# Performance work log

Measured on AMD Instinct MI355X. Metric: run time of the kernel, lower is better.

## Reference

```python
import jax, jax.numpy as jnp
import numpy as np

N_NODES = 10000
N_EDGES = 320000
N_GRAPHS = 64
IN_DIM = 1
HID = 256


def setup_inputs() -> dict:
    key = jax.random.key(0)
    ks = jax.random.split(key, 12)
    s = 1.0 / np.sqrt(HID)
    inp = {
        "x": jax.random.normal(ks[0], (N_NODES, IN_DIM), dtype=jnp.float32),
        "edge_index": jax.random.randint(ks[1], (2, N_EDGES), 0, N_NODES, dtype=jnp.int64),
        "batch": jnp.sort(jax.random.randint(ks[2], (N_NODES,), 0, N_GRAPHS, dtype=jnp.int64)),
        "W_emb": jax.random.normal(ks[3], (IN_DIM, HID), dtype=jnp.float32),
        "b_emb": jnp.zeros((HID,), dtype=jnp.float32),
        "W1a": jax.random.normal(ks[4], (HID, HID), dtype=jnp.float32) * s,
        "b1a": jnp.zeros((HID,), dtype=jnp.float32),
        "W1b": jax.random.normal(ks[5], (HID, HID), dtype=jnp.float32) * s,
        "b1b": jnp.zeros((HID,), dtype=jnp.float32),
        "W2a": jax.random.normal(ks[6], (HID, HID), dtype=jnp.float32) * s,
        "b2a": jnp.zeros((HID,), dtype=jnp.float32),
        "W2b": jax.random.normal(ks[7], (HID, HID), dtype=jnp.float32) * s,
        "b2b": jnp.zeros((HID,), dtype=jnp.float32),
    }
    return inp


def _pointnet_conv(h, src, dst, Wa, ba, Wb, bb):
    # gather x_j -> 2-layer MLP per edge -> scatter-max at dst (PyG aggr='max')
    msg = jax.nn.relu(h[src] @ Wa + ba) @ Wb + bb          # [E, HID]
    agg = jax.ops.segment_max(msg, dst, num_segments=N_NODES)
    # PyG fills nodes with no incoming messages with 0
    return jnp.where(jnp.isneginf(agg), 0.0, agg)


def reference(x, edge_index, batch, W_emb, b_emb, W1a, b1a, W1b, b1b, W2a, b2a, W2b, b2b):
    src, dst = edge_index[0], edge_index[1]
    h = jax.nn.silu(x @ W_emb + b_emb)                     # [N, HID]
    h = h + jax.nn.silu(_pointnet_conv(h, src, dst, W1a, b1a, W1b, b1b))
    h = h + jax.nn.silu(_pointnet_conv(h, src, dst, W2a, b2a, W2b, b2b))
    # global_mean_pool over graphs
    sums = jax.ops.segment_sum(h, batch, num_segments=N_GRAPHS)          # [G, HID]
    cnts = jax.ops.segment_sum(jnp.ones((h.shape[0],), h.dtype), batch, num_segments=N_GRAPHS)
    return sums / jnp.maximum(cnts, 1.0)[:, None]
```

## Files before the change

kernel.cpp:

```cpp
#include <hip/hip_runtime.h>
#include <hip/hip_bf16.h>
#include <math.h>

#define HID 256
#define CAP 128

typedef __attribute__((ext_vector_type(8))) short bf16x8;
typedef __attribute__((ext_vector_type(8))) unsigned short u16x8;
typedef __attribute__((ext_vector_type(4))) float f32x4;

__device__ __forceinline__ float silu_f(float z) {
    return z / (1.0f + __expf(-z));
}
__device__ __forceinline__ unsigned short f2bf(float f) {
    unsigned int u = __float_as_uint(f);
    u = (u + 0x7FFFu + ((u >> 16) & 1u)) >> 16;
    return (unsigned short)u;
}
__device__ __forceinline__ float bf2f(unsigned short b) {
    return __uint_as_float(((unsigned int)b) << 16);
}
__device__ __forceinline__ void max8(float m[8], u16x8 v) {
#pragma unroll
    for (int k = 0; k < 8; ++k) m[k] = fmaxf(m[k], bf2f(v[k]));
}

__global__ __launch_bounds__(256) void k_prep(
    const float* __restrict__ w0, const float* __restrict__ w1,
    const float* __restrict__ w2, const float* __restrict__ w3,
    unsigned short* __restrict__ o0, unsigned short* __restrict__ o1,
    unsigned short* __restrict__ o2, unsigned short* __restrict__ o3,
    int* __restrict__ cnt,
    const int* __restrict__ batch, int* __restrict__ goff,
    int N, int G) {
    __shared__ float ls[64][65];
    int b = blockIdx.x;
    int tid = threadIdx.x;
    if (b < 64) {
        int mat = b >> 4;
        int tile = b & 15;
        int k0 = (tile >> 2) * 64;
        int n0 = (tile & 3) * 64;
        const float* in = (mat == 0) ? w0 : (mat == 1) ? w1 : (mat == 2) ? w2 : w3;
        unsigned short* op = (mat == 0) ? o0 : (mat == 1) ? o1 : (mat == 2) ? o2 : o3;
        int lrb = tid >> 4;
        int lc = (tid & 15) * 4;
#pragma unroll
        for (int p = 0; p < 4; ++p) {
            int lr = p * 16 + lrb;
            float4 v = *(const float4*)(in + (size_t)(k0 + lr) * HID + n0 + lc);
            ls[lr][lc + 0] = v.x; ls[lr][lc + 1] = v.y;
            ls[lr][lc + 2] = v.z; ls[lr][lc + 3] = v.w;
        }
        __syncthreads();
#pragma unroll
        for (int p = 0; p < 4; ++p) {
            int ln = p * 16 + lrb;
            ushort4 q;
            q.x = f2bf(ls[lc + 0][ln]);
            q.y = f2bf(ls[lc + 1][ln]);
            q.z = f2bf(ls[lc + 2][ln]);
            q.w = f2bf(ls[lc + 3][ln]);
            *(ushort4*)(op + (size_t)(n0 + ln) * HID + k0 + lc) = q;
        }
    } else if (b == 64) {
        int g = tid;
        if (g > G) return;
        int lo = 0, hi = N;
        while (lo < hi) {
            int mid = (lo + hi) >> 1;
            if (batch[mid] < g) lo = mid + 1; else hi = mid;
        }
        goff[g] = lo;
    } else {
        int i = (b - 65) * 256 + tid;
        if (i < N) cnt[i] = 0;
    }
}

__global__ __launch_bounds__(256) void k_mlp1f(
    const float* __restrict__ x, const float* __restrict__ Wemb,
    const float* __restrict__ bemb,
    const unsigned short* __restrict__ Wta, const float* __restrict__ ba,
    const unsigned short* __restrict__ Wtb, const float* __restrict__ bbv,
    unsigned short* __restrict__ hb, unsigned short* __restrict__ t2,
    const int* __restrict__ src, const int* __restrict__ dst,
    int* __restrict__ cnt, int* __restrict__ csr,
    int M, int E, int MT) {
    __shared__ unsigned short As[32][264];
    __shared__ unsigned short t1s[32][264];
    int b = blockIdx.x;
    int tid = threadIdx.x;

    if (b >= MT) {
        int e = (b - MT) * 256 + tid;
        if (e < E) {
            int d = dst[e];
            int p = atomicAdd(&cnt[d], 1);
            if (p < CAP) csr[d * CAP + p] = src[e];
        }
        return;
    }

    int lane = tid & 63;
    int wave = tid >> 6;
    int quad = lane >> 4;
    int r = lane & 15;
    int m0 = b * 32;
    int colw = wave * 64;

    {
        int row = tid >> 3;
        int c0 = (tid & 7) * 32;
        int grow = m0 + row;
        float xv = (grow < M) ? x[grow] : 0.0f;
#pragma unroll
        for (int j = 0; j < 8; ++j) {
            int c = c0 + j * 4;
            ushort4 q;
            q.x = f2bf(silu_f(xv * Wemb[c + 0] + bemb[c + 0]));
            q.y = f2bf(silu_f(xv * Wemb[c + 1] + bemb[c + 1]));
            q.z = f2bf(silu_f(xv * Wemb[c + 2] + bemb[c + 2]));
            q.w = f2bf(silu_f(xv * Wemb[c + 3] + bemb[c + 3]));
            if (grow < M) *(ushort4*)(hb + (size_t)grow * HID + c) = q;
            *(ushort4*)&As[row][c] = q;
        }
        __syncthreads();
    }

    f32x4 acc[2][4];
#pragma unroll
    for (int rt = 0; rt < 2; ++rt)
#pragma unroll
        for (int nt = 0; nt < 4; ++nt) acc[rt][nt] = (f32x4)0.0f;
#pragma unroll
    for (int ks = 0; ks < 8; ++ks) {
        bf16x8 a0 = *(const bf16x8*)&As[r][ks * 32 + quad * 8];
        bf16x8 a1 = *(const bf16x8*)&As[r + 16][ks * 32 + quad * 8];
#pragma unroll
        for (int nt = 0; nt < 4; ++nt) {
            bf16x8 bfr = *(const bf16x8*)(Wta + (size_t)(colw + nt * 16 + r) * HID
                                          + ks * 32 + quad * 8);
            acc[0][nt] = __builtin_amdgcn_mfma_f32_16x16x32_bf16(a0, bfr, acc[0][nt], 0, 0, 0);
            acc[1][nt] = __builtin_amdgcn_mfma_f32_16x16x32_bf16(a1, bfr, acc[1][nt], 0, 0, 0);
        }
    }
#pragma unroll
    for (int nt = 0; nt < 4; ++nt) {
        int col = colw + nt * 16 + r;
        float bv = ba[col];
#pragma unroll
        for (int rt = 0; rt < 2; ++rt)
#pragma unroll
            for (int i = 0; i < 4; ++i) {
                float v = fmaxf(acc[rt][nt][i] + bv, 0.0f);
                t1s[rt * 16 + quad * 4 + i][col] = f2bf(v);
            }
    }
    __syncthreads();

    f32x4 acc2[2][4];
#pragma unroll
    for (int rt = 0; rt < 2; ++rt)
#pragma unroll
        for (int nt = 0; nt < 4; ++nt) acc2[rt][nt] = (f32x4)0.0f;
#pragma unroll
    for (int ks = 0; ks < 8; ++ks) {
        bf16x8 a0 = *(const bf16x8*)&t1s[r][ks * 32 + quad * 8];
        bf16x8 a1 = *(const bf16x8*)&t1s[r + 16][ks * 32 + quad * 8];
#pragma unroll
        for (int nt = 0; nt < 4; ++nt) {
            bf16x8 bfr = *(const bf16x8*)(Wtb + (size_t)(colw + nt * 16 + r) * HID
                                          + ks * 32 + quad * 8);
            acc2[0][nt] = __builtin_amdgcn_mfma_f32_16x16x32_bf16(a0, bfr, acc2[0][nt], 0, 0, 0);
            acc2[1][nt] = __builtin_amdgcn_mfma_f32_16x16x32_bf16(a1, bfr, acc2[1][nt], 0, 0, 0);
        }
    }
#pragma unroll
    for (int nt = 0; nt < 4; ++nt) {
        int col = colw + nt * 16 + r;
        float bv = bbv[col];
#pragma unroll
        for (int rt = 0; rt < 2; ++rt)
#pragma unroll
            for (int i = 0; i < 4; ++i) {
                int row = m0 + rt * 16 + quad * 4 + i;
                if (row < M) t2[(size_t)row * HID + col] = f2bf(acc2[rt][nt][i] + bv);
            }
    }
}

__global__ __launch_bounds__(256) void k_mlp2(
    const unsigned short* __restrict__ Aglob,
    const unsigned short* __restrict__ Wta, const float* __restrict__ ba,
    const unsigned short* __restrict__ Wtb, const float* __restrict__ bbv,
    unsigned short* __restrict__ t2, int M) {
    __shared__ unsigned short t1s[32][264];
    int tid = threadIdx.x;
    int lane = tid & 63;
    int wave = tid >> 6;
    int quad = lane >> 4;
    int r = lane & 15;
    int m0 = blockIdx.x * 32;
    int colw = wave * 64;

    f32x4 acc[2][4];
#pragma unroll
    for (int rt = 0; rt < 2; ++rt)
#pragma unroll
        for (int nt = 0; nt < 4; ++nt) acc[rt][nt] = (f32x4)0.0f;

    int ar0 = m0 + r;        if (ar0 >= M) ar0 = M - 1;
    int ar1 = m0 + 16 + r;   if (ar1 >= M) ar1 = M - 1;

#pragma unroll
    for (int ks = 0; ks < 8; ++ks) {
        bf16x8 a0 = *(const bf16x8*)(Aglob + (size_t)ar0 * HID + ks * 32 + quad * 8);
        bf16x8 a1 = *(const bf16x8*)(Aglob + (size_t)ar1 * HID + ks * 32 + quad * 8);
#pragma unroll
        for (int nt = 0; nt < 4; ++nt) {
            bf16x8 bfr = *(const bf16x8*)(Wta + (size_t)(colw + nt * 16 + r) * HID
                                          + ks * 32 + quad * 8);
            acc[0][nt] = __builtin_amdgcn_mfma_f32_16x16x32_bf16(a0, bfr, acc[0][nt], 0, 0, 0);
            acc[1][nt] = __builtin_amdgcn_mfma_f32_16x16x32_bf16(a1, bfr, acc[1][nt], 0, 0, 0);
        }
    }
#pragma unroll
    for (int nt = 0; nt < 4; ++nt) {
        int col = colw + nt * 16 + r;
        float bv = ba[col];
#pragma unroll
        for (int rt = 0; rt < 2; ++rt)
#pragma unroll
            for (int i = 0; i < 4; ++i) {
                float v = fmaxf(acc[rt][nt][i] + bv, 0.0f);
                t1s[rt * 16 + quad * 4 + i][col] = f2bf(v);
            }
    }
    __syncthreads();

    f32x4 acc2[2][4];
#pragma unroll
    for (int rt = 0; rt < 2; ++rt)
#pragma unroll
        for (int nt = 0; nt < 4; ++nt) acc2[rt][nt] = (f32x4)0.0f;
#pragma unroll
    for (int ks = 0; ks < 8; ++ks) {
        bf16x8 a0 = *(const bf16x8*)&t1s[r][ks * 32 + quad * 8];
        bf16x8 a1 = *(const bf16x8*)&t1s[r + 16][ks * 32 + quad * 8];
#pragma unroll
        for (int nt = 0; nt < 4; ++nt) {
            bf16x8 bfr = *(const bf16x8*)(Wtb + (size_t)(colw + nt * 16 + r) * HID
                                          + ks * 32 + quad * 8);
            acc2[0][nt] = __builtin_amdgcn_mfma_f32_16x16x32_bf16(a0, bfr, acc2[0][nt], 0, 0, 0);
            acc2[1][nt] = __builtin_amdgcn_mfma_f32_16x16x32_bf16(a1, bfr, acc2[1][nt], 0, 0, 0);
        }
    }
#pragma unroll
    for (int nt = 0; nt < 4; ++nt) {
        int col = colw + nt * 16 + r;
        float bv = bbv[col];
#pragma unroll
        for (int rt = 0; rt < 2; ++rt)
#pragma unroll
            for (int i = 0; i < 4; ++i) {
                int row = m0 + rt * 16 + quad * 4 + i;
                if (row < M) t2[(size_t)row * HID + col] = f2bf(acc2[rt][nt][i] + bv);
            }
    }
}

__global__ __launch_bounds__(256) void k_agg(const unsigned short* __restrict__ t2,
                                             const int* __restrict__ cnt,
                                             const int* __restrict__ csr,
                                             unsigned short* __restrict__ hb, int N) {
    int lane = threadIdx.x & 63;
    int node = (blockIdx.x * blockDim.x + threadIdx.x) >> 6;
    if (node >= N) return;
    int half = lane >> 5;
    int lc = (lane & 31) * 8;
    const unsigned short* base = t2 + lc;

    int deg = cnt[node];
    if (deg > CAP) deg = CAP;
    const int* rowp = csr + (size_t)node * CAP;
    size_t o = (size_t)node * HID + lc;
    u16x8 hq = *(const u16x8*)(hb + o);

    float m[8];
#pragma unroll
    for (int k = 0; k < 8; ++k) m[k] = -INFINITY;

    int i = 0;
    for (; i + 16 <= deg; i += 16) {
        int s[8];
#pragma unroll
        for (int j = 0; j < 8; ++j) s[j] = rowp[i + 2 * j + half];
        u16x8 v[8];
#pragma unroll
        for (int j = 0; j < 8; ++j) v[j] = *(const u16x8*)(base + (size_t)s[j] * HID);
#pragma unroll
        for (int j = 0; j < 8; ++j) max8(m, v[j]);
    }
    if (i + 8 <= deg) {
        int s[4];
#pragma unroll
        for (int j = 0; j < 4; ++j) s[j] = rowp[i + 2 * j + half];
        u16x8 v[4];
#pragma unroll
        for (int j = 0; j < 4; ++j) v[j] = *(const u16x8*)(base + (size_t)s[j] * HID);
#pragma unroll
        for (int j = 0; j < 4; ++j) max8(m, v[j]);
        i += 8;
    }
    for (; i < deg; i += 2) {
        int idx = i + half; if (idx >= deg) idx = deg - 1;
        int s = rowp[idx];
        u16x8 v = *(const u16x8*)(base + (size_t)s * HID);
        max8(m, v);
    }

#pragma unroll
    for (int k = 0; k < 8; ++k) m[k] = fmaxf(m[k], __shfl_xor(m[k], 32, 64));
    if (deg == 0) {
#pragma unroll
        for (int k = 0; k < 8; ++k) m[k] = 0.0f;
    }

    if (half == 0) {
        u16x8 q;
#pragma unroll
        for (int k = 0; k < 8; ++k) q[k] = f2bf(bf2f(hq[k]) + silu_f(m[k]));
        *(u16x8*)(hb + o) = q;
    }
}

__global__ __launch_bounds__(1024) void k_pool(const unsigned short* __restrict__ hb,
                                               const int* __restrict__ goff,
                                               float* __restrict__ out) {
    __shared__ float part[3][HID];
    int g = blockIdx.x;
    int tid = threadIdx.x;
    int c = tid & 255;
    int chunk = tid >> 8;
    int beg = goff[g], end = goff[g + 1];
    float s = 0.f;
    for (int n = beg + chunk; n < end; n += 4) s += bf2f(hb[(size_t)n * HID + c]);
    if (chunk > 0) part[chunk - 1][c] = s;
    __syncthreads();
    if (chunk == 0) {
        s += part[0][c] + part[1][c] + part[2][c];
        int cnt = end - beg;
        out[g * HID + c] = s / (float)(cnt > 0 ? cnt : 1);
    }
}

extern "C" void kernel_launch(void* const* d_in, const int* in_sizes, int n_in,
                              void* d_out, int out_size, void* d_ws, size_t ws_size,
                              hipStream_t stream) {
    const float* x     = (const float*)d_in[0];
    const int*   ei    = (const int*)d_in[1];
    const int*   batch = (const int*)d_in[2];
    const float* Wemb  = (const float*)d_in[3];
    const float* bemb  = (const float*)d_in[4];
    const float* W1a   = (const float*)d_in[5];
    const float* b1a   = (const float*)d_in[6];
    const float* W1b   = (const float*)d_in[7];
    const float* b1b   = (const float*)d_in[8];
    const float* W2a   = (const float*)d_in[9];
    const float* b2a   = (const float*)d_in[10];
    const float* W2b   = (const float*)d_in[11];
    const float* b2b   = (const float*)d_in[12];
    float* out = (float*)d_out;

    const int N = in_sizes[0];
    const int E = in_sizes[1] / 2;
    const int G = out_size / HID;
    const int* src = ei;
    const int* dst = ei + E;

    char* ws = (char*)d_ws;
    unsigned short* hb   = (unsigned short*)ws; ws += (size_t)N * HID * 2;
    unsigned short* t2   = (unsigned short*)ws; ws += (size_t)N * HID * 2;
    unsigned short* Wt1a = (unsigned short*)ws; ws += (size_t)HID * HID * 2;
    unsigned short* Wt1b = (unsigned short*)ws; ws += (size_t)HID * HID * 2;
    unsigned short* Wt2a = (unsigned short*)ws; ws += (size_t)HID * HID * 2;
    unsigned short* Wt2b = (unsigned short*)ws; ws += (size_t)HID * HID * 2;
    int* cnt  = (int*)ws; ws += (size_t)N * 4;
    int* goff = (int*)ws; ws += (size_t)(G + 1) * 4;
    int* csr  = (int*)ws; ws += (size_t)N * CAP * 4;

    const int nh = (E + 255) / 256;
    const int nz = (N + 255) / 256;
    const int MT = (N + 31) / 32;

    k_prep<<<64 + 1 + nz, 256, 0, stream>>>(W1a, W1b, W2a, W2b,
                                            Wt1a, Wt1b, Wt2a, Wt2b,
                                            cnt, batch, goff, N, G);

    k_mlp1f<<<MT + nh, 256, 0, stream>>>(x, Wemb, bemb, Wt1a, b1a, Wt1b, b1b,
                                         hb, t2, src, dst, cnt, csr, N, E, MT);

    int agg_blocks = (N * 64 + 255) / 256;

    k_agg<<<agg_blocks, 256, 0, stream>>>(t2, cnt, csr, hb, N);

    k_mlp2<<<MT, 256, 0, stream>>>(hb, Wt2a, b2a, Wt2b, b2b, t2, N);

    k_agg<<<agg_blocks, 256, 0, stream>>>(t2, cnt, csr, hb, N);

    k_pool<<<G, 1024, 0, stream>>>(hb, goff, out);
}
```

Baseline: 202.5 us.

## Shard per-node edge counters four ways and widen agg lanes

The CSR build now spreads each destination's atomic counter over four shards chosen by edge index. Each shard owns 32 slots of the node's 128-slot row, which cuts atomic contention on hot nodes. The aggregation kernel switches from two half-waves of 8 bf16 each to all 64 lanes of 4 bf16 each. It walks the four shards in lockstep, which removes the cross-half shuffle reduction. The trade-off is that per-shard capacity drops to 32, so a skewed node can lose edges even when its total degree is under 128, and the gather vectors are narrower.

```diff
diff --git a/kernel.cpp b/kernel.cpp
--- a/kernel.cpp
+++ b/kernel.cpp
@@ -4,9 +4,9 @@
 
 #define HID 256
 #define CAP 128
+#define SLOTS 32
 
 typedef __attribute__((ext_vector_type(8))) short bf16x8;
-typedef __attribute__((ext_vector_type(8))) unsigned short u16x8;
 typedef __attribute__((ext_vector_type(4))) float f32x4;
 
 __device__ __forceinline__ float silu_f(float z) {
@@ -20,9 +20,11 @@
 __device__ __forceinline__ float bf2f(unsigned short b) {
     return __uint_as_float(((unsigned int)b) << 16);
 }
-__device__ __forceinline__ void max8(float m[8], u16x8 v) {
-#pragma unroll
-    for (int k = 0; k < 8; ++k) m[k] = fmaxf(m[k], bf2f(v[k]));
+__device__ __forceinline__ void max4(float4& m, ushort4 v) {
+    m.x = fmaxf(m.x, bf2f(v.x));
+    m.y = fmaxf(m.y, bf2f(v.y));
+    m.z = fmaxf(m.z, bf2f(v.z));
+    m.w = fmaxf(m.w, bf2f(v.w));
 }
 
 __global__ __launch_bounds__(256) void k_prep(
@@ -74,7 +76,7 @@
         goff[g] = lo;
     } else {
         int i = (b - 65) * 256 + tid;
-        if (i < N) cnt[i] = 0;
+        if (i < 4 * N) cnt[i] = 0;
     }
 }
 
@@ -96,8 +98,9 @@
         int e = (b - MT) * 256 + tid;
         if (e < E) {
             int d = dst[e];
-            int p = atomicAdd(&cnt[d], 1);
-            if (p < CAP) csr[d * CAP + p] = src[e];
+            int sh = e & 3;
+            int p = atomicAdd(&cnt[sh * M + d], 1);
+            if (p < SLOTS) csr[(size_t)d * CAP + sh * SLOTS + p] = src[e];
         }
         return;
     }
@@ -277,62 +280,62 @@
     int lane = threadIdx.x & 63;
     int node = (blockIdx.x * blockDim.x + threadIdx.x) >> 6;
     if (node >= N) return;
-    int half = lane >> 5;
-    int lc = (lane & 31) * 8;
-    const unsigned short* base = t2 + lc;
-
-    int deg = cnt[node];
-    if (deg > CAP) deg = CAP;
+    const unsigned short* base = t2 + lane * 4;
+
+    int cs[4];
+#pragma unroll
+    for (int q = 0; q < 4; ++q) {
+        int c = cnt[q * N + node];
+        cs[q] = (c > SLOTS) ? SLOTS : c;
+    }
+    int deg = cs[0] + cs[1] + cs[2] + cs[3];
+    int minc = min(min(cs[0], cs[1]), min(cs[2], cs[3]));
     const int* rowp = csr + (size_t)node * CAP;
-    size_t o = (size_t)node * HID + lc;
-    u16x8 hq = *(const u16x8*)(hb + o);
-
-    float m[8];
-#pragma unroll
-    for (int k = 0; k < 8; ++k) m[k] = -INFINITY;
-
-    int i = 0;
-    for (; i + 16 <= deg; i += 16) {
+    size_t o = (size_t)node * HID + lane * 4;
+    ushort4 hq = *(const ushort4*)(hb + o);
+
+    float4 m = make_float4(-INFINITY, -INFINITY, -INFINITY, -INFINITY);
+    int t = 0;
+    for (; t + 2 <= minc; t += 2) {
         int s[8];
 #pragma unroll
-        for (int j = 0; j < 8; ++j) s[j] = rowp[i + 2 * j + half];
-        u16x8 v[8];
-#pragma unroll
-        for (int j = 0; j < 8; ++j) v[j] = *(const u16x8*)(base + (size_t)s[j] * HID);
-#pragma unroll
-        for (int j = 0; j < 8; ++j) max8(m, v[j]);
-    }
-    if (i + 8 <= deg) {
+        for (int q = 0; q < 4; ++q) {
+            s[q]     = rowp[q * SLOTS + t];
+            s[4 + q] = rowp[q * SLOTS + t + 1];
+        }
+        ushort4 v[8];
+#pragma unroll
+        for (int j = 0; j < 8; ++j) v[j] = *(const ushort4*)(base + (size_t)s[j] * HID);
+#pragma unroll
+        for (int j = 0; j < 8; ++j) max4(m, v[j]);
+    }
+    if (t < minc) {
         int s[4];
 #pragma unroll
-        for (int j = 0; j < 4; ++j) s[j] = rowp[i + 2 * j + half];
-        u16x8 v[4];
-#pragma unroll
-        for (int j = 0; j < 4; ++j) v[j] = *(const u16x8*)(base + (size_t)s[j] * HID);
-#pragma unroll
-        for (int j = 0; j < 4; ++j) max8(m, v[j]);
-        i += 8;
-    }
-    for (; i < deg; i += 2) {
-        int idx = i + half; if (idx >= deg) idx = deg - 1;
-        int s = rowp[idx];
-        u16x8 v = *(const u16x8*)(base + (size_t)s * HID);
-        max8(m, v);
-    }
-
-#pragma unroll
-    for (int k = 0; k < 8; ++k) m[k] = fmaxf(m[k], __shfl_xor(m[k], 32, 64));
-    if (deg == 0) {
-#pragma unroll
-        for (int k = 0; k < 8; ++k) m[k] = 0.0f;
-    }
-
-    if (half == 0) {
-        u16x8 q;
-#pragma unroll
-        for (int k = 0; k < 8; ++k) q[k] = f2bf(bf2f(hq[k]) + silu_f(m[k]));
-        *(u16x8*)(hb + o) = q;
-    }
+        for (int q = 0; q < 4; ++q) s[q] = rowp[q * SLOTS + t];
+        ushort4 v[4];
+#pragma unroll
+        for (int j = 0; j < 4; ++j) v[j] = *(const ushort4*)(base + (size_t)s[j] * HID);
+#pragma unroll
+        for (int j = 0; j < 4; ++j) max4(m, v[j]);
+        ++t;
+    }
+#pragma unroll
+    for (int q = 0; q < 4; ++q) {
+        for (int j = t; j < cs[q]; ++j) {
+            int s = rowp[q * SLOTS + j];
+            ushort4 v = *(const ushort4*)(base + (size_t)s * HID);
+            max4(m, v);
+        }
+    }
+    if (deg == 0) m = make_float4(0.f, 0.f, 0.f, 0.f);
+
+    ushort4 q;
+    q.x = f2bf(bf2f(hq.x) + silu_f(m.x));
+    q.y = f2bf(bf2f(hq.y) + silu_f(m.y));
+    q.z = f2bf(bf2f(hq.z) + silu_f(m.z));
+    q.w = f2bf(bf2f(hq.w) + silu_f(m.w));
+    *(ushort4*)(hb + o) = q;
 }
 
 __global__ __launch_bounds__(1024) void k_pool(const unsigned short* __restrict__ hb,
@@ -386,12 +389,12 @@
     unsigned short* Wt1b = (unsigned short*)ws; ws += (size_t)HID * HID * 2;
     unsigned short* Wt2a = (unsigned short*)ws; ws += (size_t)HID * HID * 2;
     unsigned short* Wt2b = (unsigned short*)ws; ws += (size_t)HID * HID * 2;
-    int* cnt  = (int*)ws; ws += (size_t)N * 4;
+    int* cnt  = (int*)ws; ws += (size_t)4 * N * 4;
     int* goff = (int*)ws; ws += (size_t)(G + 1) * 4;
     int* csr  = (int*)ws; ws += (size_t)N * CAP * 4;
 
     const int nh = (E + 255) / 256;
-    const int nz = (N + 255) / 256;
+    const int nz = (4 * N + 255) / 256;
     const int MT = (N + 31) / 32;
 
     k_prep<<<64 + 1 + nz, 256, 0, stream>>>(W1a, W1b, W2a, W2b,
```

Result: slower. 224.0 us (+10.6%).
